# Kernel tuning notes

Measured on AMD Instinct MI355X. Metric: run time of the kernel, lower is better.

The kernel has to match this reference:

```python
import jax, jax.numpy as jnp
import numpy as np

D = 1024      # d_model
H = 16        # n_heads
DH = 64       # d_head
K = 4         # conv_kernel
C = H * DH    # channels for depthwise convs


def setup_inputs() -> dict:
    key = jax.random.key(0)
    ks = jax.random.split(key, 16)
    s = 0.02
    w = lambda k, shape: (jax.random.normal(k, shape, jnp.float32) * s)
    return {
        'hidden_states': jax.random.normal(ks[0], (4, 2048, D), jnp.float32),
        'Wq': w(ks[1], (C, D)),
        'Wk': w(ks[2], (C, D)),
        'Wv': w(ks[3], (C, D)),
        'Wa': w(ks[4], (H, D)), 'ba': jnp.zeros((H,), jnp.float32),
        'Wb': w(ks[5], (H, D)), 'bb': jnp.zeros((H,), jnp.float32),
        'conv_q_w': w(ks[6], (C, 1, K)), 'conv_q_b': jnp.zeros((C,), jnp.float32),
        'conv_k_w': w(ks[7], (C, 1, K)), 'conv_k_b': jnp.zeros((C,), jnp.float32),
        'conv_v_w': w(ks[8], (C, 1, K)), 'conv_v_b': jnp.zeros((C,), jnp.float32),
        'Wg': w(ks[9], (C, D)), 'bg': jnp.zeros((C,), jnp.float32),
        'Wo': w(ks[10], (D, C)),
    }


def _causal_conv(x, w, b):
    # x: (B, C, T); depthwise causal conv (torch pads K-1 both sides then slices [:T])
    y = jax.lax.conv_general_dilated(
        x, w, window_strides=(1,), padding=[(K - 1, 0)],
        feature_group_count=C, dimension_numbers=('NCH', 'OIH', 'NCH'))
    return y + b[None, :, None]


def reference(hidden_states, Wq, Wk, Wv, Wa, ba, Wb, bb,
              conv_q_w, conv_q_b, conv_k_w, conv_k_b, conv_v_w, conv_v_b,
              Wg, bg, Wo):
    B, T, _ = hidden_states.shape
    # projections -> (B, C, T) for conv
    q = jnp.einsum('btd,cd->bct', hidden_states, Wq)
    k = jnp.einsum('btd,cd->bct', hidden_states, Wk)
    v = jnp.einsum('btd,cd->bct', hidden_states, Wv)
    q = jax.nn.silu(_causal_conv(q, conv_q_w, conv_q_b))
    k = jax.nn.silu(_causal_conv(k, conv_k_w, conv_k_b))
    v = jax.nn.silu(_causal_conv(v, conv_v_w, conv_v_b))
    # (B, T, H, DH)
    q = q.transpose(0, 2, 1).reshape(B, T, H, DH)
    k = k.transpose(0, 2, 1).reshape(B, T, H, DH)
    v = v.transpose(0, 2, 1).reshape(B, T, H, DH)
    # F.normalize(k, p=2, dim=-1)
    k = k / jnp.maximum(jnp.linalg.norm(k, axis=-1, keepdims=True), 1e-12)
    alpha = jax.nn.sigmoid(jnp.einsum('btd,hd->bth', hidden_states, Wa) + ba)
    beta = jax.nn.sigmoid(jnp.einsum('btd,hd->bth', hidden_states, Wb) + bb)

    def step(S, xs):
        kt, vt, qt, at, bt = xs            # (B,H,DH) x3, (B,H) x2
        v_old = jnp.einsum('bhij,bhj->bhi', S, kt)
        upd = vt - at[..., None] * v_old   # (B,H,DH)
        dS = upd[..., :, None] * kt[..., None, :]
        S = jnp.clip(at[..., None, None] * S + bt[..., None, None] * dS, -5.0, 5.0)
        ot = jnp.einsum('bhij,bhj->bhi', S, qt)
        return S, ot

    S0 = jnp.zeros((B, H, DH, DH), hidden_states.dtype)
    xs = (k.transpose(1, 0, 2, 3), v.transpose(1, 0, 2, 3), q.transpose(1, 0, 2, 3),
          alpha.transpose(1, 0, 2), beta.transpose(1, 0, 2))
    _, ys = jax.lax.scan(step, S0, xs)     # ys: (T, B, H, DH)
    y = ys.transpose(1, 0, 2, 3).reshape(B, T, C)
    g = jax.nn.silu(jnp.einsum('btd,cd->btc', hidden_states, Wg) + bg)
    y = y * g
    out = jnp.einsum('btc,dc->btd', y, Wo)
    return out
```

## Files before the change

### kernel.cpp

```cpp
#include <hip/hip_runtime.h>
#include <cstdint>
#include <cstddef>

#define TSEQ 2048
#define NB   4
#define NH   16
#define MM   (NB * TSEQ)
#define KK   1024
#define NCAT 4224

typedef __attribute__((ext_vector_type(8))) __bf16 bf16x8;
typedef __attribute__((ext_vector_type(4))) float f32x4;
typedef __attribute__((ext_vector_type(4))) int   int4v;

__device__ __forceinline__ unsigned short f2bf(float f) {
  unsigned int u = __float_as_uint(f);
  u += 0x7fffu + ((u >> 16) & 1u);
  return (unsigned short)(u >> 16);
}
__device__ __forceinline__ float bf2f(unsigned short h) {
  return __uint_as_float(((unsigned int)h) << 16);
}
__device__ __forceinline__ float sigmoidf_(float x) { return 1.0f / (1.0f + expf(-x)); }
__device__ __forceinline__ float siluf_(float x)    { return x / (1.0f + expf(-x)); }

__device__ __forceinline__ uint32_t packsplit(float x) {
  unsigned short h = f2bf(x);
  unsigned short l = f2bf(x - bf2f(h));
  return ((uint32_t)h << 16) | (uint32_t)l;
}

union BF8 { bf16x8 v; unsigned short s[8]; };

__device__ __forceinline__ void frag_from_packed(const uint32_t* p, bf16x8& hi, bf16x8& lo) {
  int4v a = *(const int4v*)p;
  int4v b = *(const int4v*)(p + 4);
  BF8 H, L;
#pragma unroll
  for (int e = 0; e < 4; ++e) {
    uint32_t ua = ((const uint32_t*)&a)[e];
    uint32_t ub = ((const uint32_t*)&b)[e];
    H.s[e]     = (unsigned short)(ua >> 16);
    L.s[e]     = (unsigned short)(ua & 0xffffu);
    H.s[e + 4] = (unsigned short)(ub >> 16);
    L.s[e + 4] = (unsigned short)(ub & 0xffffu);
  }
  hi = H.v; lo = L.v;
}

__device__ __forceinline__ f32x4 mfma3(bf16x8 ah, bf16x8 al, bf16x8 bh, bf16x8 bl, f32x4 acc) {
  acc = __builtin_amdgcn_mfma_f32_16x16x32_bf16(ah, bh, acc, 0, 0, 0);
  acc = __builtin_amdgcn_mfma_f32_16x16x32_bf16(ah, bl, acc, 0, 0, 0);
  acc = __builtin_amdgcn_mfma_f32_16x16x32_bf16(al, bh, acc, 0, 0, 0);
  return acc;
}

__global__ void k_split(const float* __restrict__ x, unsigned short* __restrict__ hi,
                        unsigned short* __restrict__ lo, int n) {
  int idx = blockIdx.x * blockDim.x + threadIdx.x;
  if (idx >= n) return;
  float v = x[idx];
  unsigned short h = f2bf(v);
  hi[idx] = h;
  lo[idx] = f2bf(v - bf2f(h));
}

__global__ void k_build_wcat(const float* __restrict__ Wq, const float* __restrict__ Wk,
                             const float* __restrict__ Wv, const float* __restrict__ Wg,
                             const float* __restrict__ Wa, const float* __restrict__ Wb,
                             unsigned short* __restrict__ hi, unsigned short* __restrict__ lo) {
  int idx = blockIdx.x * blockDim.x + threadIdx.x;
  if (idx >= NCAT * KK) return;
  int row = idx >> 10, col = idx & 1023;
  float v = 0.0f;
  if      (row < 1024) v = Wq[idx];
  else if (row < 2048) v = Wk[idx - 1024 * 1024];
  else if (row < 3072) v = Wv[idx - 2048 * 1024];
  else if (row < 4096) v = Wg[idx - 3072 * 1024];
  else if (row < 4112) v = Wa[(row - 4096) * 1024 + col];
  else if (row < 4128) v = Wb[(row - 4112) * 1024 + col];
  unsigned short h = f2bf(v);
  hi[idx] = h;
  lo[idx] = f2bf(v - bf2f(h));
}

__global__ __launch_bounds__(256, 2)
void k_gemm(const unsigned short* __restrict__ Ahi, const unsigned short* __restrict__ Alo,
            const unsigned short* __restrict__ Bhi, const unsigned short* __restrict__ Blo,
            int Kdim, int mode,
            float* __restrict__ Qb, float* __restrict__ Kb, float* __restrict__ Vb,
            float* __restrict__ Gb, float* __restrict__ Ab, float* __restrict__ Bbuf,
            const float* __restrict__ bg, const float* __restrict__ ba, const float* __restrict__ bb,
            float* __restrict__ Out) {
  __shared__ __align__(16) unsigned short As_hi[128 * 32];
  __shared__ __align__(16) unsigned short As_lo[128 * 32];
  __shared__ __align__(16) unsigned short Bs_hi[128 * 32];
  __shared__ __align__(16) unsigned short Bs_lo[128 * 32];

  const int tid  = threadIdx.x;
  const int lane = tid & 63;
  const int l15  = lane & 15;
  const int quad = lane >> 4;
  const int wid  = tid >> 6;
  const int wm   = (wid >> 1) * 64;
  const int wn   = (wid & 1) * 64;
  const int m0   = blockIdx.x * 128;
  const int n0   = blockIdx.y * 128;
  const int srow = tid >> 2;
  const int skc  = (tid & 3) * 8;

  f32x4 acc[4][4];
  f32x4 zero4 = {0.f, 0.f, 0.f, 0.f};
#pragma unroll
  for (int i = 0; i < 4; ++i)
#pragma unroll
    for (int j = 0; j < 4; ++j) acc[i][j] = zero4;

  const unsigned short* pa0 = Ahi + (size_t)(m0 + srow) * Kdim + skc;
  const unsigned short* pa1 = Ahi + (size_t)(m0 + srow + 64) * Kdim + skc;
  const unsigned short* pa2 = Alo + (size_t)(m0 + srow) * Kdim + skc;
  const unsigned short* pa3 = Alo + (size_t)(m0 + srow + 64) * Kdim + skc;
  const unsigned short* pb0 = Bhi + (size_t)(n0 + srow) * Kdim + skc;
  const unsigned short* pb1 = Bhi + (size_t)(n0 + srow + 64) * Kdim + skc;
  const unsigned short* pb2 = Blo + (size_t)(n0 + srow) * Kdim + skc;
  const unsigned short* pb3 = Blo + (size_t)(n0 + srow + 64) * Kdim + skc;

  for (int kt = 0; kt < Kdim; kt += 32) {
    int4v va0 = *(const int4v*)(pa0 + kt);
    int4v va1 = *(const int4v*)(pa1 + kt);
    int4v va2 = *(const int4v*)(pa2 + kt);
    int4v va3 = *(const int4v*)(pa3 + kt);
    int4v vb0 = *(const int4v*)(pb0 + kt);
    int4v vb1 = *(const int4v*)(pb1 + kt);
    int4v vb2 = *(const int4v*)(pb2 + kt);
    int4v vb3 = *(const int4v*)(pb3 + kt);
    __syncthreads();
    *(int4v*)&As_hi[srow * 32 + skc]        = va0;
    *(int4v*)&As_hi[(srow + 64) * 32 + skc] = va1;
    *(int4v*)&As_lo[srow * 32 + skc]        = va2;
    *(int4v*)&As_lo[(srow + 64) * 32 + skc] = va3;
    *(int4v*)&Bs_hi[srow * 32 + skc]        = vb0;
    *(int4v*)&Bs_hi[(srow + 64) * 32 + skc] = vb1;
    *(int4v*)&Bs_lo[srow * 32 + skc]        = vb2;
    *(int4v*)&Bs_lo[(srow + 64) * 32 + skc] = vb3;
    __syncthreads();

    bf16x8 ah[4], al[4], bh[4], bl[4];
#pragma unroll
    for (int f = 0; f < 4; ++f) {
      int ra = (wm + f * 16 + l15) * 32 + quad * 8;
      ah[f] = *(const bf16x8*)&As_hi[ra];
      al[f] = *(const bf16x8*)&As_lo[ra];
      int rb = (wn + f * 16 + l15) * 32 + quad * 8;
      bh[f] = *(const bf16x8*)&Bs_hi[rb];
      bl[f] = *(const bf16x8*)&Bs_lo[rb];
    }
#pragma unroll
    for (int mf = 0; mf < 4; ++mf)
#pragma unroll
      for (int nf = 0; nf < 4; ++nf) {
        acc[mf][nf] = __builtin_amdgcn_mfma_f32_16x16x32_bf16(ah[mf], bh[nf], acc[mf][nf], 0, 0, 0);
        acc[mf][nf] = __builtin_amdgcn_mfma_f32_16x16x32_bf16(ah[mf], bl[nf], acc[mf][nf], 0, 0, 0);
        acc[mf][nf] = __builtin_amdgcn_mfma_f32_16x16x32_bf16(al[mf], bh[nf], acc[mf][nf], 0, 0, 0);
      }
  }

#pragma unroll
  for (int mf = 0; mf < 4; ++mf) {
    int rowb = m0 + wm + mf * 16 + quad * 4;
#pragma unroll
    for (int nf = 0; nf < 4; ++nf) {
      int col = n0 + wn + nf * 16 + l15;
      f32x4 v = acc[mf][nf];
      if (mode == 1) {
#pragma unroll
        for (int r = 0; r < 4; ++r) Out[(size_t)(rowb + r) * 1024 + col] = v[r];
      } else {
        if (col < 1024) {
#pragma unroll
          for (int r = 0; r < 4; ++r) Qb[(size_t)(rowb + r) * 1024 + col] = v[r];
        } else if (col < 2048) {
          int c = col - 1024;
#pragma unroll
          for (int r = 0; r < 4; ++r) Kb[(size_t)(rowb + r) * 1024 + c] = v[r];
        } else if (col < 3072) {
          int c = col - 2048;
#pragma unroll
          for (int r = 0; r < 4; ++r) Vb[(size_t)(rowb + r) * 1024 + c] = v[r];
        } else if (col < 4096) {
          int c = col - 3072;
          float bgc = bg[c];
#pragma unroll
          for (int r = 0; r < 4; ++r) {
            float x = v[r] + bgc;
            Gb[(size_t)(rowb + r) * 1024 + c] = siluf_(x);
          }
        } else if (col < 4112) {
          int c = col - 4096;
          float bac = ba[c];
#pragma unroll
          for (int r = 0; r < 4; ++r) Ab[(size_t)(rowb + r) * 16 + c] = sigmoidf_(v[r] + bac);
        } else if (col < 4128) {
          int c = col - 4112;
          float bbc = bb[c];
#pragma unroll
          for (int r = 0; r < 4; ++r) Bbuf[(size_t)(rowb + r) * 16 + c] = sigmoidf_(v[r] + bbc);
        }
      }
    }
  }
}

__global__ __launch_bounds__(256)
void k_intra(const float* __restrict__ Qb, const float* __restrict__ Kb,
             const float* __restrict__ Vb,
             const float* __restrict__ Ab, const float* __restrict__ Bb,
             const float* __restrict__ cqw, const float* __restrict__ cqb,
             const float* __restrict__ ckw, const float* __restrict__ ckb,
             const float* __restrict__ cvw, const float* __restrict__ cvb,
             uint32_t* __restrict__ A1buf, unsigned short* __restrict__ Qefbuf,
             unsigned short* __restrict__ G1buf, unsigned short* __restrict__ G2Tbuf,
             float* __restrict__ gCbuf) {
  __shared__ __align__(16) unsigned short Khi[64][72], Klo[64][72];
  __shared__ __align__(16) unsigned short Qhi[64][72], Qlo[64][72];
  __shared__ float Vf[64][65];
  __shared__ float Rf[64][65];
  __shared__ float Mm[64][68];
  __shared__ __align__(16) unsigned short Atthi[64][72];
  __shared__ __align__(16) uint32_t u0T[64][68], RTp[64][68];
  __shared__ __align__(16) unsigned short KwThi[64][72], KwTlo[64][72];
  __shared__ float lgs[64], gas[64], bss[64], wvs[64], ins[64];

  const int tid  = threadIdx.x;
  const int lane = tid & 63;
  const int w    = tid >> 6;
  const int l15  = lane & 15;
  const int quad = lane >> 4;
  const int bid  = blockIdx.x;
  const int c    = bid & 31;
  const int h    = (bid >> 5) & 15;
  const int b    = bid >> 9;
  const size_t ci = (size_t)bid;
  const int t0   = c * 64;
  const long rowBase = (long)b * 2048 + t0;
  const int ch   = h * 64 + lane;
  const f32x4 z4 = {0.f, 0.f, 0.f, 0.f};

  {
    long gr = (rowBase + lane) * 16 + h;
    float av = Ab[gr], bv = Bb[gr];
    float x = log2f(av);
#pragma unroll
    for (int off = 1; off < 64; off <<= 1) {
      float y = __shfl_up(x, off);
      if (lane >= off) x += y;
    }
    float l63 = __shfl(x, 63);
    lgs[lane] = x;
    gas[lane] = exp2f(x);
    bss[lane] = bv;
    wvs[lane] = exp2f(l63 - x) * bv;
  }

  {
    const float kc0 = ckw[ch * 4], kc1 = ckw[ch * 4 + 1], kc2 = ckw[ch * 4 + 2], kc3 = ckw[ch * 4 + 3], kcbv = ckb[ch];
    const float qc0 = cqw[ch * 4], qc1 = cqw[ch * 4 + 1], qc2 = cqw[ch * 4 + 2], qc3 = cqw[ch * 4 + 3], qcbv = cqb[ch];
    const float vc0 = cvw[ch * 4], vc1 = cvw[ch * 4 + 1], vc2 = cvw[ch * 4 + 2], vc3 = cvw[ch * 4 + 3], vcbv = cvb[ch];
    const int tb = t0 + w * 16;
    float kw0, kw1, kw2, qw0, qw1, qw2, vw0, vw1, vw2;
    {
      float kx[3], qx[3], vx[3];
#pragma unroll
      for (int d = 0; d < 3; ++d) {
        int tt = tb - 3 + d;
        float a = 0.f, bq = 0.f, cv = 0.f;
        if (tt >= 0) {
          long ro = ((long)b * 2048 + tt) * 1024 + ch;
          a = Kb[ro]; bq = Qb[ro]; cv = Vb[ro];
        }
        kx[d] = a; qx[d] = bq; vx[d] = cv;
      }
      kw0 = kx[0]; kw1 = kx[1]; kw2 = kx[2];
      qw0 = qx[0]; qw1 = qx[1]; qw2 = qx[2];
      vw0 = vx[0]; vw1 = vx[1]; vw2 = vx[2];
    }
#pragma unroll
    for (int lt = 0; lt < 16; ++lt) {
      const int s = w * 16 + lt;
      const long ro = (rowBase + s) * 1024 + ch;
      float kr = Kb[ro], qr = Qb[ro], vr = Vb[ro];
      float kcv = kcbv + kc0 * kw0 + kc1 * kw1 + kc2 * kw2 + kc3 * kr;
      float qcv = qcbv + qc0 * qw0 + qc1 * qw1 + qc2 * qw2 + qc3 * qr;
      float vcv = vcbv + vc0 * vw0 + vc1 * vw1 + vc2 * vw2 + vc3 * vr;
      kw0 = kw1; kw1 = kw2; kw2 = kr;
      qw0 = qw1; qw1 = qw2; qw2 = qr;
      vw0 = vw1; vw1 = vw2; vw2 = vr;
      float kv = siluf_(kcv), qv = siluf_(qcv), vv = siluf_(vcv);
      uint32_t kp_ = packsplit(kv);
      uint32_t qp_ = packsplit(qv);
      Khi[s][lane] = (unsigned short)(kp_ >> 16); Klo[s][lane] = (unsigned short)(kp_ & 0xffffu);
      Qhi[s][lane] = (unsigned short)(qp_ >> 16); Qlo[s][lane] = (unsigned short)(qp_ & 0xffffu);
      Vf[s][lane] = vv;
    }
  }
  __syncthreads();

  f32x4 accM[4], accA[4];
#pragma unroll
  for (int nt = 0; nt < 4; ++nt) { accM[nt] = z4; accA[nt] = z4; }
#pragma unroll
  for (int ks = 0; ks < 2; ++ks) {
    bf16x8 kah = *(const bf16x8*)&Khi[w * 16 + l15][ks * 32 + quad * 8];
    bf16x8 kal = *(const bf16x8*)&Klo[w * 16 + l15][ks * 32 + quad * 8];
    bf16x8 qah = *(const bf16x8*)&Qhi[w * 16 + l15][ks * 32 + quad * 8];
    bf16x8 qal = *(const bf16x8*)&Qlo[w * 16 + l15][ks * 32 + quad * 8];
#pragma unroll
    for (int nt = 0; nt < 4; ++nt) {
      bf16x8 bh = *(const bf16x8*)&Khi[nt * 16 + l15][ks * 32 + quad * 8];
      bf16x8 bl = *(const bf16x8*)&Klo[nt * 16 + l15][ks * 32 + quad * 8];
      accM[nt] = mfma3(kah, kal, bh, bl, accM[nt]);
      accA[nt] = mfma3(qah, qal, bh, bl, accA[nt]);
    }
  }
#pragma unroll
  for (int nt = 0; nt < 4; ++nt)
    if (nt == w) {
#pragma unroll
      for (int r = 0; r < 4; ++r)
        if (l15 == quad * 4 + r) ins[nt * 16 + l15] = rsqrtf(fmaxf(accM[nt][r], 1e-24f));
    }
  __syncthreads();

  {
#pragma unroll
    for (int nt = 0; nt < 4; ++nt) {
      int sc = nt * 16 + l15;
      float insc = ins[sc], lgc = lgs[sc], bsc = bss[sc];
#pragma unroll
      for (int r = 0; r < 4; ++r) {
        int sr = w * 16 + quad * 4 + r;
        Mm[sr][sc] = (sc < sr) ? exp2f(lgs[sr] - lgc) * bsc * ins[sr] * insc * accM[nt][r] : 0.f;
        Atthi[sr][sc] = f2bf((sc <= sr) ? exp2f(lgs[sr] - lgc) * bsc * insc * accA[nt][r] : 0.f);
      }
    }
    int s = w * 16 + (lane & 15);
    int jb = (lane >> 4) * 16;
    float rsc = gas[s] * ins[s];
    float wsc = wvs[s] * ins[s];
    BF8 H0, L0, H1, L1;
    H0.v = *(const bf16x8*)&Khi[s][jb];     L0.v = *(const bf16x8*)&Klo[s][jb];
    H1.v = *(const bf16x8*)&Khi[s][jb + 8]; L1.v = *(const bf16x8*)&Klo[s][jb + 8];
#pragma unroll
    for (int e = 0; e < 8; ++e) {
      float kv0 = bf2f(H0.s[e]) + bf2f(L0.s[e]);
      float kv1 = bf2f(H1.s[e]) + bf2f(L1.s[e]);
      Rf[s][jb + e]     = kv0 * rsc;
      Rf[s][jb + 8 + e] = kv1 * rsc;
      uint32_t p0 = packsplit(kv0 * wsc), p1 = packsplit(kv1 * wsc);
      KwThi[jb + e][s]     = (unsigned short)(p0 >> 16);
      KwTlo[jb + e][s]     = (unsigned short)(p0 & 0xffffu);
      KwThi[jb + 8 + e][s] = (unsigned short)(p1 >> 16);
      KwTlo[jb + 8 + e][s] = (unsigned short)(p1 & 0xffffu);
    }
  }
  if (tid == 0) gCbuf[ci] = gas[63];
  __syncthreads();

  if (w < 2) {
    float* RHS = (w == 0) ? &Vf[0][0] : &Rf[0][0];
    const int i = lane;
    float u[64];
#pragma unroll
    for (int d = 0; d < 4; ++d) {
      const int base = d * 16;
#pragma unroll
      for (int r2 = 0; r2 < 16; ++r2) {
        const int s = base + r2;
        float acc = RHS[s * 65 + i];
#pragma unroll
        for (int r = 0; r < r2; ++r) acc = fmaf(-Mm[s][base + r], u[base + r], acc);
        u[s] = acc;
        RHS[s * 65 + i] = acc;
      }
      if (d < 3) {
#pragma unroll 1
        for (int s = base + 16; s < 64; ++s) {
          f32x4 m0 = *(const f32x4*)&Mm[s][base];
          f32x4 m1 = *(const f32x4*)&Mm[s][base + 4];
          f32x4 m2 = *(const f32x4*)&Mm[s][base + 8];
          f32x4 m3 = *(const f32x4*)&Mm[s][base + 12];
          float a0 = m0[0] * u[base + 0] + m0[1] * u[base + 1] + m0[2] * u[base + 2] + m0[3] * u[base + 3];
          float a1 = m1[0] * u[base + 4] + m1[1] * u[base + 5] + m1[2] * u[base + 6] + m1[3] * u[base + 7];
          float a2 = m2[0] * u[base + 8] + m2[1] * u[base + 9] + m2[2] * u[base + 10] + m2[3] * u[base + 11];
          float a3 = m3[0] * u[base + 12] + m3[1] * u[base + 13] + m3[2] * u[base + 14] + m3[3] * u[base + 15];
          RHS[s * 65 + i] = RHS[s * 65 + i] - ((a0 + a1) + (a2 + a3));
        }
      }
    }
  }
  __syncthreads();

#pragma unroll
  for (int r = 0; r < 16; ++r) {
    int i = w * 16 + r;
    u0T[i][lane] = packsplit(Vf[lane][i]);
    RTp[i][lane] = packsplit(Rf[lane][i]);
  }
  __syncthreads();

  {
    f32x4 acc[4];
#pragma unroll
    for (int nt = 0; nt < 4; ++nt) acc[nt] = z4;
#pragma unroll
    for (int ks = 0; ks < 2; ++ks) {
      bf16x8 ta = *(const bf16x8*)&Atthi[w * 16 + l15][ks * 32 + quad * 8];
#pragma unroll
      for (int nt = 0; nt < 4; ++nt) {
        bf16x8 uh, ul;
        frag_from_packed(&u0T[nt * 16 + l15][ks * 32 + quad * 8], uh, ul);
        acc[nt] = __builtin_amdgcn_mfma_f32_16x16x32_bf16(ta, uh, acc[nt], 0, 0, 0);
        acc[nt] = __builtin_amdgcn_mfma_f32_16x16x32_bf16(ta, ul, acc[nt], 0, 0, 0);
      }
    }
#pragma unroll
    for (int nt = 0; nt < 4; ++nt)
#pragma unroll
      for (int r = 0; r < 4; ++r) {
        int t = w * 16 + quad * 4 + r, i = nt * 16 + l15;
        A1buf[ci * 4096 + t * 64 + i] = packsplit(acc[nt][r]);
      }
  }
  {
    f32x4 acc[4];
#pragma unroll
    for (int nt = 0; nt < 4; ++nt) acc[nt] = z4;
#pragma unroll
    for (int ks = 0; ks < 2; ++ks) {
      bf16x8 ta = *(const bf16x8*)&Atthi[w * 16 + l15][ks * 32 + quad * 8];
#pragma unroll
      for (int nt = 0; nt < 4; ++nt) {
        bf16x8 rh, rl;
        frag_from_packed(&RTp[nt * 16 + l15][ks * 32 + quad * 8], rh, rl);
        acc[nt] = __builtin_amdgcn_mfma_f32_16x16x32_bf16(ta, rh, acc[nt], 0, 0, 0);
        acc[nt] = __builtin_amdgcn_mfma_f32_16x16x32_bf16(ta, rl, acc[nt], 0, 0, 0);
      }
    }
#pragma unroll
    for (int nt = 0; nt < 4; ++nt)
#pragma unroll
      for (int r = 0; r < 4; ++r) {
        int t = w * 16 + quad * 4 + r, j = nt * 16 + l15;
        float q = bf2f(Qhi[t][j]) + bf2f(Qlo[t][j]);
        Qefbuf[ci * 4096 + t * 64 + j] = f2bf(gas[t] * q - acc[nt][r]);
      }
  }
  {
    f32x4 acc[4];
#pragma unroll
    for (int nt = 0; nt < 4; ++nt) acc[nt] = z4;
#pragma unroll
    for (int ks = 0; ks < 2; ++ks) {
      bf16x8 uh, ul;
      frag_from_packed(&u0T[w * 16 + l15][ks * 32 + quad * 8], uh, ul);
#pragma unroll
      for (int nt = 0; nt < 4; ++nt) {
        bf16x8 kh = *(const bf16x8*)&KwThi[nt * 16 + l15][ks * 32 + quad * 8];
        bf16x8 kl = *(const bf16x8*)&KwTlo[nt * 16 + l15][ks * 32 + quad * 8];
        acc[nt] = mfma3(uh, ul, kh, kl, acc[nt]);
      }
    }
#pragma unroll
    for (int nt = 0; nt < 4; ++nt)
#pragma unroll
      for (int r = 0; r < 4; ++r) {
        int i = w * 16 + quad * 4 + r, j = nt * 16 + l15;
        G1buf[ci * 4096 + i * 64 + j] = f2bf(acc[nt][r]);
      }
  }
  {
    f32x4 acc[4];
#pragma unroll
    for (int nt = 0; nt < 4; ++nt) acc[nt] = z4;
#pragma unroll
    for (int ks = 0; ks < 2; ++ks) {
      bf16x8 rh, rl;
      frag_from_packed(&RTp[w * 16 + l15][ks * 32 + quad * 8], rh, rl);
#pragma unroll
      for (int nt = 0; nt < 4; ++nt) {
        bf16x8 kh = *(const bf16x8*)&KwThi[nt * 16 + l15][ks * 32 + quad * 8];
        bf16x8 kl = *(const bf16x8*)&KwTlo[nt * 16 + l15][ks * 32 + quad * 8];
        acc[nt] = mfma3(rh, rl, kh, kl, acc[nt]);
      }
    }
#pragma unroll
    for (int nt = 0; nt < 4; ++nt) {
      int j = nt * 16 + l15;
      int mb = w * 16 + quad * 4;
      uint32_t lo32 = (uint32_t)f2bf(acc[nt][0]) | ((uint32_t)f2bf(acc[nt][1]) << 16);
      uint32_t hi32 = (uint32_t)f2bf(acc[nt][2]) | ((uint32_t)f2bf(acc[nt][3]) << 16);
      uint32_t* dst = (uint32_t*)&G2Tbuf[ci * 4096 + j * 64 + mb];
      dst[0] = lo32; dst[1] = hi32;
    }
  }
}

__global__ __launch_bounds__(256)
void k_serial(const uint32_t* __restrict__ A1buf, const unsigned short* __restrict__ Qefbuf,
              const unsigned short* __restrict__ G1buf, const unsigned short* __restrict__ G2Tbuf,
              const float* __restrict__ gCbuf, const float* __restrict__ Gb,
              unsigned short* __restrict__ Yhi, unsigned short* __restrict__ Ylo) {
  __shared__ uint32_t A1L[64][66];
  __shared__ __align__(16) unsigned short QefL[64][72], G1L[64][72], G2TL[64][72];
  __shared__ __align__(16) unsigned short S0hi[64][72], S0lo[64][72];
  __shared__ float S0f[64][65];

  const int tid  = threadIdx.x;
  const int lane = tid & 63;
  const int w    = tid >> 6;
  const int l15  = lane & 15;
  const int quad = lane >> 4;
  const int b    = blockIdx.x >> 4;
  const int h    = blockIdx.x & 15;
  const size_t bh = (size_t)blockIdx.x;
  const f32x4 z4 = {0.f, 0.f, 0.f, 0.f};

  for (int n = tid; n < 64 * 65; n += 256) (&S0f[0][0])[n] = 0.f;
  for (int n = tid; n < 64 * 72; n += 256) { (&S0hi[0][0])[n] = 0; (&S0lo[0][0])[n] = 0; }

  uint32_t rA[16], rQ[8], rG1[8], rG2[8];
  float pg[16], pgC;
  {
    const uint32_t* pA = A1buf + bh * 32 * 4096;
    const uint32_t* pQ = (const uint32_t*)Qefbuf + bh * 32 * 2048;
    const uint32_t* pG1 = (const uint32_t*)G1buf + bh * 32 * 2048;
    const uint32_t* pG2 = (const uint32_t*)G2Tbuf + bh * 32 * 2048;
#pragma unroll
    for (int k = 0; k < 16; ++k) rA[k] = pA[tid + k * 256];
#pragma unroll
    for (int k = 0; k < 8; ++k) { rQ[k] = pQ[tid + k * 256]; rG1[k] = pG1[tid + k * 256]; rG2[k] = pG2[tid + k * 256]; }
    pgC = gCbuf[bh * 32];
#pragma unroll
    for (int nt = 0; nt < 4; ++nt)
#pragma unroll
      for (int r = 0; r < 4; ++r)
        pg[nt * 4 + r] = Gb[((long)b * 2048 + w * 16 + quad * 4 + r) * 1024 + h * 64 + nt * 16 + l15];
  }
  __syncthreads();

#pragma unroll 1
  for (int c = 0; c < 32; ++c) {
#pragma unroll
    for (int k = 0; k < 16; ++k) {
      int idx = tid + k * 256;
      A1L[idx >> 6][idx & 63] = rA[k];
    }
#pragma unroll
    for (int k = 0; k < 8; ++k) {
      int i32 = tid + k * 256;
      int row = i32 >> 5, col = (i32 & 31) * 2;
      *(uint32_t*)&QefL[row][col] = rQ[k];
      *(uint32_t*)&G1L[row][col]  = rG1[k];
      *(uint32_t*)&G2TL[row][col] = rG2[k];
    }
    float gC = pgC;
    float pgl[16];
#pragma unroll
    for (int e = 0; e < 16; ++e) pgl[e] = pg[e];
    __syncthreads();

    f32x4 accO[4], accS[4];
#pragma unroll
    for (int nt = 0; nt < 4; ++nt) { accO[nt] = z4; accS[nt] = z4; }
#pragma unroll
    for (int ks = 0; ks < 2; ++ks) {
      bf16x8 qa = *(const bf16x8*)&QefL[w * 16 + l15][ks * 32 + quad * 8];
      bf16x8 sah = *(const bf16x8*)&S0hi[w * 16 + l15][ks * 32 + quad * 8];
      bf16x8 sal = *(const bf16x8*)&S0lo[w * 16 + l15][ks * 32 + quad * 8];
#pragma unroll
      for (int nt = 0; nt < 4; ++nt) {
        bf16x8 sh = *(const bf16x8*)&S0hi[nt * 16 + l15][ks * 32 + quad * 8];
        bf16x8 sl = *(const bf16x8*)&S0lo[nt * 16 + l15][ks * 32 + quad * 8];
        accO[nt] = __builtin_amdgcn_mfma_f32_16x16x32_bf16(qa, sh, accO[nt], 0, 0, 0);
        accO[nt] = __builtin_amdgcn_mfma_f32_16x16x32_bf16(qa, sl, accO[nt], 0, 0, 0);
        bf16x8 g2 = *(const bf16x8*)&G2TL[nt * 16 + l15][ks * 32 + quad * 8];
        accS[nt] = __builtin_amdgcn_mfma_f32_16x16x32_bf16(sah, g2, accS[nt], 0, 0, 0);
        accS[nt] = __builtin_amdgcn_mfma_f32_16x16x32_bf16(sal, g2, accS[nt], 0, 0, 0);
      }
    }
    {
      const int cc = (c + 1 < 32) ? c + 1 : 31;
      const uint32_t* pA = A1buf + (bh * 32 + cc) * 4096;
      const uint32_t* pQ = (const uint32_t*)Qefbuf + (bh * 32 + cc) * 2048;
      const uint32_t* pG1 = (const uint32_t*)G1buf + (bh * 32 + cc) * 2048;
      const uint32_t* pG2 = (const uint32_t*)G2Tbuf + (bh * 32 + cc) * 2048;
#pragma unroll
      for (int k = 0; k < 16; ++k) rA[k] = pA[tid + k * 256];
#pragma unroll
      for (int k = 0; k < 8; ++k) { rQ[k] = pQ[tid + k * 256]; rG1[k] = pG1[tid + k * 256]; rG2[k] = pG2[tid + k * 256]; }
      pgC = gCbuf[bh * 32 + cc];
#pragma unroll
      for (int nt = 0; nt < 4; ++nt)
#pragma unroll
        for (int r = 0; r < 4; ++r)
          pg[nt * 4 + r] = Gb[((long)b * 2048 + cc * 64 + w * 16 + quad * 4 + r) * 1024 + h * 64 + nt * 16 + l15];
    }
    __syncthreads();

#pragma unroll
    for (int nt = 0; nt < 4; ++nt)
#pragma unroll
      for (int r = 0; r < 4; ++r) {
        int t = w * 16 + quad * 4 + r, i = nt * 16 + l15;
        uint32_t a1 = A1L[t][i];
        float o = accO[nt][r] + bf2f((unsigned short)(a1 >> 16)) + bf2f((unsigned short)(a1 & 0xffffu));
        float y = o * pgl[nt * 4 + r];
        long ro = ((long)b * 2048 + c * 64 + t) * 1024 + h * 64 + i;
        unsigned short hy = f2bf(y);
        Yhi[ro] = hy;
        Ylo[ro] = f2bf(y - bf2f(hy));
      }
#pragma unroll
    for (int nt = 0; nt < 4; ++nt)
#pragma unroll
      for (int r = 0; r < 4; ++r) {
        int i = w * 16 + quad * 4 + r, j = nt * 16 + l15;
        float sn = gC * S0f[i][j] + bf2f(G1L[i][j]) - accS[nt][r];
        S0f[i][j] = sn;
        uint32_t p = packsplit(sn);
        S0hi[i][j] = (unsigned short)(p >> 16);
        S0lo[i][j] = (unsigned short)(p & 0xffffu);
      }
    __syncthreads();
  }
}

extern "C" void kernel_launch(void* const* d_in, const int* in_sizes, int n_in,
                              void* d_out, int out_size, void* d_ws, size_t ws_size,
                              hipStream_t stream) {
  const float* X   = (const float*)d_in[0];
  const float* Wq  = (const float*)d_in[1];
  const float* Wk  = (const float*)d_in[2];
  const float* Wv  = (const float*)d_in[3];
  const float* Wa  = (const float*)d_in[4];
  const float* ba  = (const float*)d_in[5];
  const float* Wb  = (const float*)d_in[6];
  const float* bb  = (const float*)d_in[7];
  const float* cqw = (const float*)d_in[8];
  const float* cqb = (const float*)d_in[9];
  const float* ckw = (const float*)d_in[10];
  const float* ckb = (const float*)d_in[11];
  const float* cvw = (const float*)d_in[12];
  const float* cvb = (const float*)d_in[13];
  const float* Wg  = (const float*)d_in[14];
  const float* bg  = (const float*)d_in[15];
  const float* Wo  = (const float*)d_in[16];
  float* Out = (float*)d_out;

  char* ws = (char*)d_ws;
  size_t off = 0;
  auto alloc = [&](size_t bytes) -> void* {
    void* p = ws + off;
    off += (bytes + 255) & ~(size_t)255;
    return p;
  };
  unsigned short* Xhi = (unsigned short*)alloc((size_t)MM * KK * 2);
  unsigned short* Xlo = (unsigned short*)alloc((size_t)MM * KK * 2);
  unsigned short* Whi = (unsigned short*)alloc((size_t)NCAT * KK * 2);
  unsigned short* Wlo = (unsigned short*)alloc((size_t)NCAT * KK * 2);
  float* Qb  = (float*)alloc((size_t)MM * 1024 * 4);
  float* Kb  = (float*)alloc((size_t)MM * 1024 * 4);
  float* Vb  = (float*)alloc((size_t)MM * 1024 * 4);
  float* Ab  = (float*)alloc((size_t)MM * 16 * 4);
  float* Bbf = (float*)alloc((size_t)MM * 16 * 4);
  uint32_t*       A1buf  = (uint32_t*)alloc((size_t)2048 * 4096 * 4);
  unsigned short* G1buf  = (unsigned short*)alloc((size_t)2048 * 4096 * 2);
  unsigned short* G2Tbuf = (unsigned short*)alloc((size_t)2048 * 4096 * 2);
  float*          gCbuf  = (float*)alloc((size_t)2048 * 4);
  float* Gb = Out;
  unsigned short* Yhi = Xhi;
  unsigned short* Ylo = Xlo;
  unsigned short* Qefbuf = Whi;
  unsigned short* Wohi = Whi;
  unsigned short* Wolo = Wlo;

  const int nX = MM * KK;
  k_split<<<(nX + 255) / 256, 256, 0, stream>>>(X, Xhi, Xlo, nX);
  k_build_wcat<<<(NCAT * KK + 255) / 256, 256, 0, stream>>>(Wq, Wk, Wv, Wg, Wa, Wb, Whi, Wlo);
  k_gemm<<<dim3(MM / 128, NCAT / 128), 256, 0, stream>>>(
      Xhi, Xlo, Whi, Wlo, KK, 0, Qb, Kb, Vb, Gb, Ab, Bbf, bg, ba, bb, nullptr);
  k_intra<<<NB * NH * 32, 256, 0, stream>>>(Qb, Kb, Vb, Ab, Bbf,
                                            cqw, cqb, ckw, ckb, cvw, cvb,
                                            A1buf, Qefbuf, G1buf, G2Tbuf, gCbuf);
  k_serial<<<NB * NH, 256, 0, stream>>>(A1buf, Qefbuf, G1buf, G2Tbuf, gCbuf, Gb, Yhi, Ylo);
  k_split<<<(1024 * 1024 + 255) / 256, 256, 0, stream>>>(Wo, Wohi, Wolo, 1024 * 1024);
  k_gemm<<<dim3(MM / 128, 1024 / 128), 256, 0, stream>>>(
      Yhi, Ylo, Wohi, Wolo, KK, 1, nullptr, nullptr, nullptr, nullptr, nullptr, nullptr,
      nullptr, nullptr, nullptr, Out);
}
```

Before: 718.4 us.

## Use direct global-to-LDS loads in GEMM and shrink k_intra shared memory

The projection GEMM now stages tiles into LDS with global_load_lds instead of loading through registers and storing. k_intra aliases several shared buffers, keeps the triangular-solve vectors in registers instead of LDS, and asks for two blocks per CU via launch bounds. It also drops the low half of the KwT split-bf16 operand, which removes one MFMA per product but lowers precision. The packed-fragment reader switches to 8-byte loads to match the new 66-word row stride.

```diff
diff --git a/kernel.cpp b/kernel.cpp
--- a/kernel.cpp
+++ b/kernel.cpp
@@ -12,6 +12,7 @@
 typedef __attribute__((ext_vector_type(8))) __bf16 bf16x8;
 typedef __attribute__((ext_vector_type(4))) float f32x4;
 typedef __attribute__((ext_vector_type(4))) int   int4v;
+typedef __attribute__((ext_vector_type(2))) int   int2v;
 
 __device__ __forceinline__ unsigned short f2bf(float f) {
   unsigned int u = __float_as_uint(f);
@@ -32,18 +33,21 @@
 
 union BF8 { bf16x8 v; unsigned short s[8]; };
 
-__device__ __forceinline__ void frag_from_packed(const uint32_t* p, bf16x8& hi, bf16x8& lo) {
-  int4v a = *(const int4v*)p;
-  int4v b = *(const int4v*)(p + 4);
+__device__ __forceinline__ void frag_from_packed8(const uint32_t* p, bf16x8& hi, bf16x8& lo) {
+  int2v a = *(const int2v*)p;
+  int2v b = *(const int2v*)(p + 2);
+  int2v c = *(const int2v*)(p + 4);
+  int2v d = *(const int2v*)(p + 6);
+  uint32_t uu[8];
+  uu[0] = ((const uint32_t*)&a)[0]; uu[1] = ((const uint32_t*)&a)[1];
+  uu[2] = ((const uint32_t*)&b)[0]; uu[3] = ((const uint32_t*)&b)[1];
+  uu[4] = ((const uint32_t*)&c)[0]; uu[5] = ((const uint32_t*)&c)[1];
+  uu[6] = ((const uint32_t*)&d)[0]; uu[7] = ((const uint32_t*)&d)[1];
   BF8 H, L;
 #pragma unroll
-  for (int e = 0; e < 4; ++e) {
-    uint32_t ua = ((const uint32_t*)&a)[e];
-    uint32_t ub = ((const uint32_t*)&b)[e];
-    H.s[e]     = (unsigned short)(ua >> 16);
-    L.s[e]     = (unsigned short)(ua & 0xffffu);
-    H.s[e + 4] = (unsigned short)(ub >> 16);
-    L.s[e + 4] = (unsigned short)(ub & 0xffffu);
+  for (int e = 0; e < 8; ++e) {
+    H.s[e] = (unsigned short)(uu[e] >> 16);
+    L.s[e] = (unsigned short)(uu[e] & 0xffffu);
   }
   hi = H.v; lo = L.v;
 }
@@ -54,6 +58,10 @@
   acc = __builtin_amdgcn_mfma_f32_16x16x32_bf16(al, bh, acc, 0, 0, 0);
   return acc;
 }
+
+#define GLDS16(gp, lp) __builtin_amdgcn_global_load_lds( \
+    (const __attribute__((address_space(1))) unsigned int*)(gp), \
+    (__attribute__((address_space(3))) unsigned int*)(lp), 16, 0, 0)
 
 __global__ void k_split(const float* __restrict__ x, unsigned short* __restrict__ hi,
                         unsigned short* __restrict__ lo, int n) {
@@ -125,24 +133,25 @@
   const unsigned short* pb2 = Blo + (size_t)(n0 + srow) * Kdim + skc;
   const unsigned short* pb3 = Blo + (size_t)(n0 + srow + 64) * Kdim + skc;
 
+  char* a0b = (char*)As_hi + wid * 1024;
+  char* a1b = (char*)As_hi + 4096 + wid * 1024;
+  char* a2b = (char*)As_lo + wid * 1024;
+  char* a3b = (char*)As_lo + 4096 + wid * 1024;
+  char* b0b = (char*)Bs_hi + wid * 1024;
+  char* b1b = (char*)Bs_hi + 4096 + wid * 1024;
+  char* b2b = (char*)Bs_lo + wid * 1024;
+  char* b3b = (char*)Bs_lo + 4096 + wid * 1024;
+
   for (int kt = 0; kt < Kdim; kt += 32) {
-    int4v va0 = *(const int4v*)(pa0 + kt);
-    int4v va1 = *(const int4v*)(pa1 + kt);
-    int4v va2 = *(const int4v*)(pa2 + kt);
-    int4v va3 = *(const int4v*)(pa3 + kt);
-    int4v vb0 = *(const int4v*)(pb0 + kt);
-    int4v vb1 = *(const int4v*)(pb1 + kt);
-    int4v vb2 = *(const int4v*)(pb2 + kt);
-    int4v vb3 = *(const int4v*)(pb3 + kt);
     __syncthreads();
-    *(int4v*)&As_hi[srow * 32 + skc]        = va0;
-    *(int4v*)&As_hi[(srow + 64) * 32 + skc] = va1;
-    *(int4v*)&As_lo[srow * 32 + skc]        = va2;
-    *(int4v*)&As_lo[(srow + 64) * 32 + skc] = va3;
-    *(int4v*)&Bs_hi[srow * 32 + skc]        = vb0;
-    *(int4v*)&Bs_hi[(srow + 64) * 32 + skc] = vb1;
-    *(int4v*)&Bs_lo[srow * 32 + skc]        = vb2;
-    *(int4v*)&Bs_lo[(srow + 64) * 32 + skc] = vb3;
+    GLDS16(pa0 + kt, a0b);
+    GLDS16(pa1 + kt, a1b);
+    GLDS16(pa2 + kt, a2b);
+    GLDS16(pa3 + kt, a3b);
+    GLDS16(pb0 + kt, b0b);
+    GLDS16(pb1 + kt, b1b);
+    GLDS16(pb2 + kt, b2b);
+    GLDS16(pb3 + kt, b3b);
     __syncthreads();
 
     bf16x8 ah[4], al[4], bh[4], bl[4];
@@ -211,7 +220,7 @@
   }
 }
 
-__global__ __launch_bounds__(256)
+__global__ __launch_bounds__(256, 2)
 void k_intra(const float* __restrict__ Qb, const float* __restrict__ Kb,
              const float* __restrict__ Vb,
              const float* __restrict__ Ab, const float* __restrict__ Bb,
@@ -221,15 +230,20 @@
              uint32_t* __restrict__ A1buf, unsigned short* __restrict__ Qefbuf,
              unsigned short* __restrict__ G1buf, unsigned short* __restrict__ G2Tbuf,
              float* __restrict__ gCbuf) {
-  __shared__ __align__(16) unsigned short Khi[64][72], Klo[64][72];
-  __shared__ __align__(16) unsigned short Qhi[64][72], Qlo[64][72];
-  __shared__ float Vf[64][65];
-  __shared__ float Rf[64][65];
-  __shared__ float Mm[64][68];
+  __shared__ __align__(16) unsigned short KK2[2][64][72];
+  __shared__ __align__(16) unsigned short QQ2[2][64][72];
+  __shared__ __align__(16) float Mm[64][68];
   __shared__ __align__(16) unsigned short Atthi[64][72];
-  __shared__ __align__(16) uint32_t u0T[64][68], RTp[64][68];
-  __shared__ __align__(16) unsigned short KwThi[64][72], KwTlo[64][72];
+  __shared__ __align__(16) unsigned short KwThi[64][72];
   __shared__ float lgs[64], gas[64], bss[64], wvs[64], ins[64];
+
+  unsigned short (*Khi)[72] = KK2[0];
+  unsigned short (*Klo)[72] = KK2[1];
+  unsigned short (*Qhi)[72] = QQ2[0];
+  unsigned short (*Qlo)[72] = QQ2[1];
+  uint32_t (*Vp)[66]  = (uint32_t (*)[66])&KK2[0][0][0];
+  uint32_t (*u0T)[66] = (uint32_t (*)[66])&KK2[0][0][0];
+  uint32_t (*RTp)[66] = (uint32_t (*)[66])&Mm[0][0];
 
   const int tid  = threadIdx.x;
   const int lane = tid & 63;
@@ -246,6 +260,9 @@
   const int ch   = h * 64 + lane;
   const f32x4 z4 = {0.f, 0.f, 0.f, 0.f};
 
+  float u[64];
+  float vvals[16];
+
   {
     long gr = (rowBase + lane) * 16 + h;
     float av = Ab[gr], bv = Bb[gr];
@@ -295,12 +312,12 @@
       kw0 = kw1; kw1 = kw2; kw2 = kr;
       qw0 = qw1; qw1 = qw2; qw2 = qr;
       vw0 = vw1; vw1 = vw2; vw2 = vr;
-      float kv = siluf_(kcv), qv = siluf_(qcv), vv = siluf_(vcv);
+      float kv = siluf_(kcv), qv = siluf_(qcv);
+      vvals[lt] = siluf_(vcv);
       uint32_t kp_ = packsplit(kv);
       uint32_t qp_ = packsplit(qv);
       Khi[s][lane] = (unsigned short)(kp_ >> 16); Klo[s][lane] = (unsigned short)(kp_ & 0xffffu);
       Qhi[s][lane] = (unsigned short)(qp_ >> 16); Qlo[s][lane] = (unsigned short)(qp_ & 0xffffu);
-      Vf[s][lane] = vv;
     }
   }
   __syncthreads();
@@ -345,7 +362,6 @@
     }
     int s = w * 16 + (lane & 15);
     int jb = (lane >> 4) * 16;
-    float rsc = gas[s] * ins[s];
     float wsc = wvs[s] * ins[s];
     BF8 H0, L0, H1, L1;
     H0.v = *(const bf16x8*)&Khi[s][jb];     L0.v = *(const bf16x8*)&Klo[s][jb];
@@ -354,57 +370,66 @@
     for (int e = 0; e < 8; ++e) {
       float kv0 = bf2f(H0.s[e]) + bf2f(L0.s[e]);
       float kv1 = bf2f(H1.s[e]) + bf2f(L1.s[e]);
-      Rf[s][jb + e]     = kv0 * rsc;
-      Rf[s][jb + 8 + e] = kv1 * rsc;
-      uint32_t p0 = packsplit(kv0 * wsc), p1 = packsplit(kv1 * wsc);
-      KwThi[jb + e][s]     = (unsigned short)(p0 >> 16);
-      KwTlo[jb + e][s]     = (unsigned short)(p0 & 0xffffu);
-      KwThi[jb + 8 + e][s] = (unsigned short)(p1 >> 16);
-      KwTlo[jb + 8 + e][s] = (unsigned short)(p1 & 0xffffu);
+      KwThi[jb + e][s]     = f2bf(kv0 * wsc);
+      KwThi[jb + 8 + e][s] = f2bf(kv1 * wsc);
+    }
+    if (w == 1) {
+#pragma unroll
+      for (int s2 = 0; s2 < 64; ++s2) {
+        float kv = bf2f(Khi[s2][lane]) + bf2f(Klo[s2][lane]);
+        u[s2] = gas[s2] * ins[s2] * kv;
+      }
     }
   }
   if (tid == 0) gCbuf[ci] = gas[63];
   __syncthreads();
 
+#pragma unroll
+  for (int lt = 0; lt < 16; ++lt) Vp[w * 16 + lt][lane] = packsplit(vvals[lt]);
+  __syncthreads();
+
+  if (w == 0) {
+#pragma unroll
+    for (int s2 = 0; s2 < 64; ++s2) {
+      uint32_t p = Vp[s2][lane];
+      u[s2] = bf2f((unsigned short)(p >> 16)) + bf2f((unsigned short)(p & 0xffffu));
+    }
+  }
   if (w < 2) {
-    float* RHS = (w == 0) ? &Vf[0][0] : &Rf[0][0];
-    const int i = lane;
-    float u[64];
 #pragma unroll
     for (int d = 0; d < 4; ++d) {
       const int base = d * 16;
 #pragma unroll
-      for (int r2 = 0; r2 < 16; ++r2) {
-        const int s = base + r2;
-        float acc = RHS[s * 65 + i];
-#pragma unroll
-        for (int r = 0; r < r2; ++r) acc = fmaf(-Mm[s][base + r], u[base + r], acc);
-        u[s] = acc;
-        RHS[s * 65 + i] = acc;
+      for (int r2 = 1; r2 < 16; ++r2) {
+        float acc = u[base + r2];
+#pragma unroll
+        for (int r = 0; r < r2; ++r) acc = fmaf(-Mm[base + r2][base + r], u[base + r], acc);
+        u[base + r2] = acc;
       }
       if (d < 3) {
-#pragma unroll 1
-        for (int s = base + 16; s < 64; ++s) {
-          f32x4 m0 = *(const f32x4*)&Mm[s][base];
-          f32x4 m1 = *(const f32x4*)&Mm[s][base + 4];
-          f32x4 m2 = *(const f32x4*)&Mm[s][base + 8];
-          f32x4 m3 = *(const f32x4*)&Mm[s][base + 12];
+#pragma unroll
+        for (int s2 = base + 16; s2 < 64; ++s2) {
+          f32x4 m0 = *(const f32x4*)&Mm[s2][base];
+          f32x4 m1 = *(const f32x4*)&Mm[s2][base + 4];
+          f32x4 m2 = *(const f32x4*)&Mm[s2][base + 8];
+          f32x4 m3 = *(const f32x4*)&Mm[s2][base + 12];
           float a0 = m0[0] * u[base + 0] + m0[1] * u[base + 1] + m0[2] * u[base + 2] + m0[3] * u[base + 3];
           float a1 = m1[0] * u[base + 4] + m1[1] * u[base + 5] + m1[2] * u[base + 6] + m1[3] * u[base + 7];
           float a2 = m2[0] * u[base + 8] + m2[1] * u[base + 9] + m2[2] * u[base + 10] + m2[3] * u[base + 11];
           float a3 = m3[0] * u[base + 12] + m3[1] * u[base + 13] + m3[2] * u[base + 14] + m3[3] * u[base + 15];
-          RHS[s * 65 + i] = RHS[s * 65 + i] - ((a0 + a1) + (a2 + a3));
+          u[s2] = u[s2] - ((a0 + a1) + (a2 + a3));
         }
       }
     }
   }
   __syncthreads();
 
-#pragma unroll
-  for (int r = 0; r < 16; ++r) {
-    int i = w * 16 + r;
-    u0T[i][lane] = packsplit(Vf[lane][i]);
-    RTp[i][lane] = packsplit(Rf[lane][i]);
+  if (w == 0) {
+#pragma unroll
+    for (int s2 = 0; s2 < 64; ++s2) u0T[lane][s2] = packsplit(u[s2]);
+  } else if (w == 1) {
+#pragma unroll
+    for (int s2 = 0; s2 < 64; ++s2) RTp[lane][s2] = packsplit(u[s2]);
   }
   __syncthreads();
 
@@ -418,7 +443,7 @@
 #pragma unroll
       for (int nt = 0; nt < 4; ++nt) {
         bf16x8 uh, ul;
-        frag_from_packed(&u0T[nt * 16 + l15][ks * 32 + quad * 8], uh, ul);
+        frag_from_packed8(&u0T[nt * 16 + l15][ks * 32 + quad * 8], uh, ul);
         acc[nt] = __builtin_amdgcn_mfma_f32_16x16x32_bf16(ta, uh, acc[nt], 0, 0, 0);
         acc[nt] = __builtin_amdgcn_mfma_f32_16x16x32_bf16(ta, ul, acc[nt], 0, 0, 0);
       }
@@ -441,7 +466,7 @@
 #pragma unroll
       for (int nt = 0; nt < 4; ++nt) {
         bf16x8 rh, rl;
-        frag_from_packed(&RTp[nt * 16 + l15][ks * 32 + quad * 8], rh, rl);
+        frag_from_packed8(&RTp[nt * 16 + l15][ks * 32 + quad * 8], rh, rl);
         acc[nt] = __builtin_amdgcn_mfma_f32_16x16x32_bf16(ta, rh, acc[nt], 0, 0, 0);
         acc[nt] = __builtin_amdgcn_mfma_f32_16x16x32_bf16(ta, rl, acc[nt], 0, 0, 0);
       }
@@ -462,12 +487,12 @@
 #pragma unroll
     for (int ks = 0; ks < 2; ++ks) {
       bf16x8 uh, ul;
-      frag_from_packed(&u0T[w * 16 + l15][ks * 32 + quad * 8], uh, ul);
+      frag_from_packed8(&u0T[w * 16 + l15][ks * 32 + quad * 8], uh, ul);
 #pragma unroll
       for (int nt = 0; nt < 4; ++nt) {
         bf16x8 kh = *(const bf16x8*)&KwThi[nt * 16 + l15][ks * 32 + quad * 8];
-        bf16x8 kl = *(const bf16x8*)&KwTlo[nt * 16 + l15][ks * 32 + quad * 8];
-        acc[nt] = mfma3(uh, ul, kh, kl, acc[nt]);
+        acc[nt] = __builtin_amdgcn_mfma_f32_16x16x32_bf16(uh, kh, acc[nt], 0, 0, 0);
+        acc[nt] = __builtin_amdgcn_mfma_f32_16x16x32_bf16(ul, kh, acc[nt], 0, 0, 0);
       }
     }
 #pragma unroll
@@ -485,12 +510,12 @@
 #pragma unroll
     for (int ks = 0; ks < 2; ++ks) {
       bf16x8 rh, rl;
-      frag_from_packed(&RTp[w * 16 + l15][ks * 32 + quad * 8], rh, rl);
+      frag_from_packed8(&RTp[w * 16 + l15][ks * 32 + quad * 8], rh, rl);
 #pragma unroll
       for (int nt = 0; nt < 4; ++nt) {
         bf16x8 kh = *(const bf16x8*)&KwThi[nt * 16 + l15][ks * 32 + quad * 8];
-        bf16x8 kl = *(const bf16x8*)&KwTlo[nt * 16 + l15][ks * 32 + quad * 8];
-        acc[nt] = mfma3(rh, rl, kh, kl, acc[nt]);
+        acc[nt] = __builtin_amdgcn_mfma_f32_16x16x32_bf16(rh, kh, acc[nt], 0, 0, 0);
+        acc[nt] = __builtin_amdgcn_mfma_f32_16x16x32_bf16(rl, kh, acc[nt], 0, 0, 0);
       }
     }
 #pragma unroll
```

Measured after the change: 1.018 ms. +41.7%, slower.
